# Performance work log

Hardware: AMD Instinct MI355X
Metric: run time of the kernel (lower is better)

The kernel has to match this reference:

```python
import jax, jax.numpy as jnp
import numpy as np

T, B, NA = 32, 32, 5          # timesteps, envs, actions
HID, FEAT = 256, 512          # lstm hidden, cnn features
IN_DIM = FEAT + NA            # lstm input size (517)
FLAT = 64 * 7 * 7             # cnn flatten size (3136)


def _conv(x, w, b, s):
    # x: NCHW, w: OIHW, VALID padding, stride s
    y = jax.lax.conv_general_dilated(x, w, (s, s), 'VALID',
                                     dimension_numbers=('NCHW', 'OIHW', 'NCHW'))
    return y + b[None, :, None, None]


def setup_inputs() -> dict:
    key = jax.random.key(0)
    ks = jax.random.split(key, 24)
    p = lambda k, shape: (jax.random.normal(k, shape, jnp.float32) * 0.05)
    return {
        'image': jax.random.uniform(ks[0], (T * B, 3, 84, 84), jnp.float32) * 255.0,
        'last_action': jax.random.randint(ks[1], (T * B,), 0, NA),
        'done': jax.random.bernoulli(ks[2], 0.05, (T * B,)).astype(jnp.float32),
        'h0': jnp.zeros((B, HID), jnp.float32),
        'c0': jnp.zeros((B, HID), jnp.float32),
        # NatureCNN params
        'W1': p(ks[3], (32, 3, 8, 8)), 'b1': jnp.zeros((32,), jnp.float32),
        'W2': p(ks[4], (64, 32, 4, 4)), 'b2': jnp.zeros((64,), jnp.float32),
        'W3': p(ks[5], (64, 64, 3, 3)), 'b3': jnp.zeros((64,), jnp.float32),
        'Wfc': p(ks[6], (FEAT, FLAT)), 'bfc': jnp.zeros((FEAT,), jnp.float32),
        # LSTM params (torch gate order i,f,g,o)
        'W_ih': p(ks[7], (4 * HID, IN_DIM)), 'W_hh': p(ks[8], (4 * HID, HID)),
        'b_ih': jnp.zeros((4 * HID,), jnp.float32), 'b_hh': jnp.zeros((4 * HID,), jnp.float32),
        # policy MLP (hidden 64, tanh)
        'Wp1': p(ks[9], (64, HID)), 'bp1': jnp.zeros((64,), jnp.float32),
        'Wp2': p(ks[10], (NA, 64)) * 0.01, 'bp2': jnp.zeros((NA,), jnp.float32),
        # value MLP
        'Wv1': p(ks[11], (64, HID)), 'bv1': jnp.zeros((64,), jnp.float32),
        'Wv2': p(ks[12], (1, 64)), 'bv2': jnp.zeros((1,), jnp.float32),
    }


def reference(image, last_action, done, h0, c0,
              W1, b1, W2, b2, W3, b3, Wfc, bfc,
              W_ih, W_hh, b_ih, b_hh,
              Wp1, bp1, Wp2, bp2, Wv1, bv1, Wv2, bv2):
    # --- extract: NatureCNN + one-hot(last_action) ---
    x = image / 255.0
    x = jax.nn.relu(_conv(x, W1, b1, 4))   # (TB,32,20,20)
    x = jax.nn.relu(_conv(x, W2, b2, 2))   # (TB,64,9,9)
    x = jax.nn.relu(_conv(x, W3, b3, 1))   # (TB,64,7,7)
    x = x.reshape(x.shape[0], -1)
    feat = jax.nn.relu(x @ Wfc.T + bfc)    # (TB,512)
    oh = jax.nn.one_hot(last_action, NA, dtype=feat.dtype)
    xs = jnp.concatenate([feat, oh], axis=1).reshape(T, B, IN_DIM)
    ds = done.reshape(T, B)

    # --- remember: done-masked LSTM recurrence (torch gate order i,f,g,o) ---
    def step(carry, inp):
        h, c = carry
        xt, dt = inp
        m = (1.0 - dt)[:, None]
        h = h * m
        c = c * m
        g = xt @ W_ih.T + b_ih + h @ W_hh.T + b_hh   # (B, 4*HID)
        i, f, gg, o = jnp.split(g, 4, axis=1)
        c = jax.nn.sigmoid(f) * c + jax.nn.sigmoid(i) * jnp.tanh(gg)
        h = jax.nn.sigmoid(o) * jnp.tanh(c)
        return (h, c), h

    (hT, cT), hs = jax.lax.scan(step, (h0, c0), (xs, ds))
    h = hs.reshape(T * B, HID)

    # --- heads ---
    logits = jnp.tanh(h @ Wp1.T + bp1) @ Wp2.T + bp2   # (TB, NA)
    v = jnp.tanh(h @ Wv1.T + bv1) @ Wv2.T + bv2        # (TB, 1)
    return logits, v, hT, cT
```

## Files before the change

kernel.cpp:

```cpp
#include <hip/hip_runtime.h>
#include <math.h>

typedef float  f4v __attribute__((ext_vector_type(4)));
typedef short  s8v __attribute__((ext_vector_type(8)));
typedef int    i4v __attribute__((ext_vector_type(4)));

__device__ __forceinline__ float sigm(float x) { return 1.f / (1.f + expf(-x)); }
__device__ __forceinline__ unsigned short f2bf(float f) {
    unsigned int u = __float_as_uint(f);
    return (unsigned short)((u + 0x7FFF + ((u >> 16) & 1)) >> 16);
}
__device__ __forceinline__ unsigned int cvt2(float lo, float hi) {
    unsigned int r;
    asm("v_cvt_pk_bf16_f32 %0, %1, %2" : "=v"(r) : "v"(lo), "v"(hi));
    return r;
}
__device__ __forceinline__ s8v pack8(float4 a, float4 b) {
    union { unsigned int u[4]; s8v v; } r;
    r.u[0] = cvt2(a.x, a.y); r.u[1] = cvt2(a.z, a.w);
    r.u[2] = cvt2(b.x, b.y); r.u[3] = cvt2(b.z, b.w);
    return r.v;
}
__device__ __forceinline__ void gload16(const void* g, void* l) {
    __builtin_amdgcn_global_load_lds((const __attribute__((address_space(1))) void*)g,
                                     (__attribute__((address_space(3))) void*)l, 16, 0, 0);
}

__global__ __launch_bounds__(256) void k_amax(const float* __restrict__ Whh,
                                              unsigned int* __restrict__ amax_bits) {
    int i = blockIdx.x * 256 + threadIdx.x;
    float v = fabsf(Whh[i]);
#pragma unroll
    for (int o = 1; o < 64; o <<= 1) v = fmaxf(v, __shfl_xor(v, o));
    if ((threadIdx.x & 63) == 0) atomicMax(amax_bits, __float_as_uint(v));
}

__global__ __launch_bounds__(256) void k_prep(const float* __restrict__ W2, const float* __restrict__ W3,
                                              const float* __restrict__ Wfc, const float* __restrict__ Wih,
                                              const float* __restrict__ W1, const float* __restrict__ Whh,
                                              const unsigned int* __restrict__ amax_bits,
                                              unsigned short* __restrict__ W2p, unsigned short* __restrict__ W3p,
                                              unsigned short* __restrict__ Wfcp, unsigned short* __restrict__ Wihp,
                                              unsigned short* __restrict__ W1p, signed char* __restrict__ Wq) {
    int i = blockIdx.x * 256 + threadIdx.x;
    if (i < 32768) {
        int co = i >> 9, k = i & 511, t = k >> 5, ci = k & 31, ky = t >> 2, kx = t & 3;
        W2p[i] = f2bf(W2[co * 512 + ci * 16 + ky * 4 + kx]);
    } else if (i < 69632) {
        int j = i - 32768;
        int co = j / 576, k = j - co * 576, t = k >> 6, ci = k & 63;
        int ky = t / 3, kx = t - ky * 3;
        W3p[j] = f2bf(W3[((co * 64 + ci) * 3 + ky) * 3 + kx]);
    } else if (i < 1675264) {
        int j = i - 69632;
        Wfcp[j] = f2bf(Wfc[j]);
    } else if (i < 2199552) {
        int j = i - 1675264;
        int n = j >> 9, k = j & 511;
        Wihp[j] = f2bf(Wih[n * 517 + k]);
    } else if (i < 2205696) {
        int j = i - 2199552;
        W1p[j] = f2bf(W1[j] * (1.f / 255.f));
    } else if (i < 2467840) {
        int j = i - 2205696;
        float amax = __uint_as_float(amax_bits[0]);
        float s = 127.f / amax;
        int qv = (int)rintf(Whh[j] * s);
        qv = qv > 127 ? 127 : (qv < -127 ? -127 : qv);
        Wq[j] = (signed char)qv;
    }
}

__global__ __launch_bounds__(256, 3) void k_conv1(const float* __restrict__ img,
                                                  const unsigned short* __restrict__ Bw,
                                                  const float* __restrict__ bias,
                                                  unsigned short* __restrict__ out) {
    __shared__ float sF[12096];
    int tid = threadIdx.x;
    int lane = tid & 63, w = tid >> 6;
    int l15 = lane & 15, q = lane >> 4;
    int bh = blockIdx.x & 1;
    int im = blockIdx.x >> 1;
    const int y0    = bh ? 40 : 0;
    const int S     = bh ? 14784 : 16128;
    const int fullc = bh ? 14 : 15;
    const int tailg = bh ? 28 : 48;
    const int t0    = bh ? 13 : 0;
    const int nt    = bh ? 12 : 13;
    char* sFb = (char*)sF;
    const char* gimg = (const char*)(img + (size_t)im * 21168);
    for (int c = 0; c < 3; ++c) {
        const char* gb = gimg + c * 28224 + y0 * 336;
        char* lb = sFb + c * S;
        for (int j = w; j < fullc; j += 4) {
            int off = j * 1024 + lane * 16;
            gload16(gb + off, lb + off);
        }
        if (w == c && lane < tailg) {
            int off = fullc * 1024 + lane * 16;
            *(float4*)(lb + off) = *(const float4*)(gb + off);
        }
    }
    const unsigned short* Bp0 = Bw + l15 * 192 + q * 8;
    const unsigned short* Bp1 = Bw + (16 + l15) * 192 + q * 8;
    s8v bf0[6], bf1[6];
#pragma unroll
    for (int ks = 0; ks < 6; ++ks) {
        bf0[ks] = *(const s8v*)(Bp0 + ks * 32);
        bf1[ks] = *(const s8v*)(Bp1 + ks * 32);
    }
    int koff[6];
#pragma unroll
    for (int ks = 0; ks < 6; ++ks) {
        int kq = ks * 4 + q;
        int c = kq >> 3, ky = kq & 7;
        koff[ks] = c * S + ky * 336;
    }
    __syncthreads();
    f4v acc[4][2];
#pragma unroll
    for (int i = 0; i < 4; ++i) { acc[i][0] = (f4v){0.f,0.f,0.f,0.f}; acc[i][1] = (f4v){0.f,0.f,0.f,0.f}; }
#pragma unroll
    for (int tt = 0; tt < 4; ++tt) {
        int li = w + tt * 4;
        if (li < nt) {
            int p = (t0 + li) * 16 + l15;
            int oy = p / 20, ox = p - oy * 20;
            int tb = (oy * 4 - y0) * 336 + ox * 16;
#pragma unroll
            for (int ks = 0; ks < 6; ++ks) {
                float4 a0 = *(const float4*)(sFb + koff[ks] + tb);
                float4 a1 = *(const float4*)(sFb + koff[ks] + tb + 16);
                s8v ua = pack8(a0, a1);
                acc[tt][0] = __builtin_amdgcn_mfma_f32_16x16x32_bf16(ua, bf0[ks], acc[tt][0], 0, 0, 0);
                acc[tt][1] = __builtin_amdgcn_mfma_f32_16x16x32_bf16(ua, bf1[ks], acc[tt][1], 0, 0, 0);
            }
        }
    }
    __syncthreads();
    unsigned short* cS = (unsigned short*)sFb;
    float b0v = bias[l15], b1v = bias[16 + l15];
#pragma unroll
    for (int tt = 0; tt < 4; ++tt) {
        int li = w + tt * 4;
        if (li < nt) {
            int pc = li * 16 + q * 4;
#pragma unroll
            for (int r = 0; r < 4; r += 2) {
                float v0 = acc[tt][0][r] + b0v;     v0 = v0 > 0.f ? v0 : 0.f;
                float v1 = acc[tt][0][r + 1] + b0v; v1 = v1 > 0.f ? v1 : 0.f;
                *(unsigned int*)&cS[l15 * 212 + pc + r] = cvt2(v0, v1);
                float u0 = acc[tt][1][r] + b1v;     u0 = u0 > 0.f ? u0 : 0.f;
                float u1 = acc[tt][1][r + 1] + b1v; u1 = u1 > 0.f ? u1 : 0.f;
                *(unsigned int*)&cS[(16 + l15) * 212 + pc + r] = cvt2(u0, u1);
            }
        }
    }
    __syncthreads();
    int hc = nt * 8;
    const unsigned int* cw = (const unsigned int*)cS;
    for (int n = w; n < 32; n += 4) {
        const unsigned int* crow = cw + n * 106;
        unsigned int* orow = (unsigned int*)(out + (im * 32 + n) * 400 + t0 * 16);
        for (int j = lane; j < hc; j += 64) orow[j] = crow[j];
    }
}

__global__ __launch_bounds__(256, 2) void k_conv2(const unsigned short* __restrict__ A,
                                                  const unsigned short* __restrict__ Bw,
                                                  const float* __restrict__ bias,
                                                  unsigned short* __restrict__ out) {
    __shared__ unsigned short sA[800 * 32];
    __shared__ unsigned short c2s[64][196];
    int tid = threadIdx.x;
    int lane = tid & 63, w = tid >> 6;
    int l15 = lane & 15, q = lane >> 4;
    int img0 = blockIdx.x * 2;
    char* sAb = (char*)sA;
    const s8v* srcv = (const s8v*)(A + img0 * 12800);
    for (int wi = tid; wi < 3200; wi += 256) {
        s8v v = srcv[wi];
        int f = wi * 8;
        int im = f / 12800, r = f - im * 12800, ci = r / 400, p = r - ci * 400;
#pragma unroll
        for (int j = 0; j < 8; ++j) {
            int R = im * 400 + p + j;
            int Rl = (R >> 1) + (R & 1) * 400;
            int by = (Rl * 32 + ci) * 2 ^ ((Rl & 7) << 4);
            *(unsigned short*)(sAb + by) = (unsigned short)v[j];
        }
    }
    __syncthreads();
    int Rb[3];
#pragma unroll
    for (int mf = 0; mf < 3; ++mf) {
        int t = w * 3 + mf;
        int im = t / 6;
        int pp = (t - im * 6) * 16 + l15;
        int px = pp > 80 ? 80 : pp;
        int oy = px / 9, ox = px - oy * 9;
        Rb[mf] = im * 400 + oy * 40 + ox * 2;
    }
    const unsigned short* Bp0 = Bw + l15 * 512 + q * 8;
    const unsigned short* Bp1 = Bw + (16 + l15) * 512 + q * 8;
    const unsigned short* Bp2 = Bw + (32 + l15) * 512 + q * 8;
    const unsigned short* Bp3 = Bw + (48 + l15) * 512 + q * 8;
    f4v acc[3][4];
#pragma unroll
    for (int i = 0; i < 3; ++i)
#pragma unroll
        for (int j = 0; j < 4; ++j) acc[i][j] = (f4v){0.f, 0.f, 0.f, 0.f};
#pragma unroll
    for (int s = 0; s < 16; ++s) {
        const int ky = s >> 2, kx = s & 3;
        const int d = ky * 20 + kx;
        s8v a[3];
#pragma unroll
        for (int mf = 0; mf < 3; ++mf) {
            int R = Rb[mf] + d;
            int Rl = (R >> 1) + (R & 1) * 400;
            int by = (Rl * 64 + q * 16) ^ ((Rl & 7) << 4);
            a[mf] = *(const s8v*)(sAb + by);
        }
        s8v b0 = *(const s8v*)(Bp0 + s * 32);
        s8v b1 = *(const s8v*)(Bp1 + s * 32);
        s8v b2 = *(const s8v*)(Bp2 + s * 32);
        s8v b3 = *(const s8v*)(Bp3 + s * 32);
#pragma unroll
        for (int mf = 0; mf < 3; ++mf) {
            acc[mf][0] = __builtin_amdgcn_mfma_f32_16x16x32_bf16(a[mf], b0, acc[mf][0], 0, 0, 0);
            acc[mf][1] = __builtin_amdgcn_mfma_f32_16x16x32_bf16(a[mf], b1, acc[mf][1], 0, 0, 0);
            acc[mf][2] = __builtin_amdgcn_mfma_f32_16x16x32_bf16(a[mf], b2, acc[mf][2], 0, 0, 0);
            acc[mf][3] = __builtin_amdgcn_mfma_f32_16x16x32_bf16(a[mf], b3, acc[mf][3], 0, 0, 0);
        }
    }
#pragma unroll
    for (int nf = 0; nf < 4; ++nf) {
        int co = nf * 16 + l15;
        float b = bias[co];
#pragma unroll
        for (int mf = 0; mf < 3; ++mf) {
            int rr = (w * 3 + mf) * 16 + q * 4;
#pragma unroll
            for (int r = 0; r < 4; r += 2) {
                float v0 = acc[mf][nf][r] + b;     v0 = v0 > 0.f ? v0 : 0.f;
                float v1 = acc[mf][nf][r + 1] + b; v1 = v1 > 0.f ? v1 : 0.f;
                *(unsigned int*)&c2s[co][rr + r] = cvt2(v0, v1);
            }
        }
    }
    __syncthreads();
    for (int idx = tid; idx < 10368; idx += 256) {
        int im = idx / 5184, r2 = idx - im * 5184, co = r2 / 81, p = r2 - co * 81;
        out[(img0 + im) * 5184 + r2] = c2s[co][im * 96 + p];
    }
}

__global__ __launch_bounds__(256, 2) void k_conv3(const unsigned short* __restrict__ A,
                                                  const unsigned short* __restrict__ Bw,
                                                  const float* __restrict__ bias,
                                                  unsigned short* __restrict__ out) {
    __shared__ unsigned short sA[162 * 64];
    __shared__ unsigned short c3s[64][132];
    int tid = threadIdx.x;
    int lane = tid & 63, w = tid >> 6;
    int l15 = lane & 15, q = lane >> 4;
    int img0 = blockIdx.x * 2;
    char* sAb = (char*)sA;
    const s8v* srcv = (const s8v*)(A + img0 * 5184);
    for (int wi = tid; wi < 1296; wi += 256) {
        s8v v = srcv[wi];
        int f = wi * 8;
#pragma unroll
        for (int j = 0; j < 8; ++j) {
            int fe = f + j;
            int im = fe / 5184, r = fe - im * 5184, ci = r / 81, p = r - ci * 81;
            int R = im * 81 + p;
            int by = (R * 64 + ci) * 2 ^ ((R & 7) << 4);
            *(unsigned short*)(sAb + by) = (unsigned short)v[j];
        }
    }
    __syncthreads();
    int Rb[2];
#pragma unroll
    for (int mf = 0; mf < 2; ++mf) {
        int t = w * 2 + mf;
        int im = t >> 2;
        int pp = (t & 3) * 16 + l15;
        int px = pp > 48 ? 48 : pp;
        int oy = px / 7, ox = px - oy * 7;
        Rb[mf] = im * 81 + oy * 9 + ox;
    }
    const unsigned short* Bp0 = Bw + l15 * 576 + q * 8;
    const unsigned short* Bp1 = Bw + (16 + l15) * 576 + q * 8;
    const unsigned short* Bp2 = Bw + (32 + l15) * 576 + q * 8;
    const unsigned short* Bp3 = Bw + (48 + l15) * 576 + q * 8;
    f4v acc[2][4];
#pragma unroll
    for (int i = 0; i < 2; ++i)
#pragma unroll
        for (int j = 0; j < 4; ++j) acc[i][j] = (f4v){0.f, 0.f, 0.f, 0.f};
#pragma unroll
    for (int s = 0; s < 18; ++s) {
        const int tap = s >> 1, cb2 = (s & 1) * 64;
        const int ky = tap / 3, kx = tap - ky * 3;
        const int d = ky * 9 + kx;
        s8v a0, a1;
        {
            int R = Rb[0] + d;
            int by = (R * 128 + cb2 + q * 16) ^ ((R & 7) << 4);
            a0 = *(const s8v*)(sAb + by);
        }
        {
            int R = Rb[1] + d;
            int by = (R * 128 + cb2 + q * 16) ^ ((R & 7) << 4);
            a1 = *(const s8v*)(sAb + by);
        }
        s8v b0 = *(const s8v*)(Bp0 + s * 32);
        s8v b1 = *(const s8v*)(Bp1 + s * 32);
        s8v b2 = *(const s8v*)(Bp2 + s * 32);
        s8v b3 = *(const s8v*)(Bp3 + s * 32);
        acc[0][0] = __builtin_amdgcn_mfma_f32_16x16x32_bf16(a0, b0, acc[0][0], 0, 0, 0);
        acc[0][1] = __builtin_amdgcn_mfma_f32_16x16x32_bf16(a0, b1, acc[0][1], 0, 0, 0);
        acc[0][2] = __builtin_amdgcn_mfma_f32_16x16x32_bf16(a0, b2, acc[0][2], 0, 0, 0);
        acc[0][3] = __builtin_amdgcn_mfma_f32_16x16x32_bf16(a0, b3, acc[0][3], 0, 0, 0);
        acc[1][0] = __builtin_amdgcn_mfma_f32_16x16x32_bf16(a1, b0, acc[1][0], 0, 0, 0);
        acc[1][1] = __builtin_amdgcn_mfma_f32_16x16x32_bf16(a1, b1, acc[1][1], 0, 0, 0);
        acc[1][2] = __builtin_amdgcn_mfma_f32_16x16x32_bf16(a1, b2, acc[1][2], 0, 0, 0);
        acc[1][3] = __builtin_amdgcn_mfma_f32_16x16x32_bf16(a1, b3, acc[1][3], 0, 0, 0);
    }
#pragma unroll
    for (int nf = 0; nf < 4; ++nf) {
        int co = nf * 16 + l15;
        float b = bias[co];
#pragma unroll
        for (int mf = 0; mf < 2; ++mf) {
            int rr = (w * 2 + mf) * 16 + q * 4;
#pragma unroll
            for (int r = 0; r < 4; r += 2) {
                float v0 = acc[mf][nf][r] + b;     v0 = v0 > 0.f ? v0 : 0.f;
                float v1 = acc[mf][nf][r + 1] + b; v1 = v1 > 0.f ? v1 : 0.f;
                *(unsigned int*)&c3s[co][rr + r] = cvt2(v0, v1);
            }
        }
    }
    __syncthreads();
    for (int idx = tid; idx < 6272; idx += 256) {
        int im = idx / 3136, r2 = idx - im * 3136, co = r2 / 49, p = r2 - co * 49;
        out[(img0 + im) * 3136 + r2] = c3s[co][im * 64 + p];
    }
}

__global__ __launch_bounds__(256) void k_fc(const unsigned short* __restrict__ A,
                                            const unsigned short* __restrict__ Bw,
                                            const float* __restrict__ bias,
                                            unsigned short* __restrict__ out) {
    int lane = threadIdx.x & 63, w = threadIdx.x >> 6;
    int l15 = lane & 15, q = lane >> 4;
    int m0 = blockIdx.x * 32 + (w & 1) * 16;
    int n0 = blockIdx.y * 64 + (w >> 1) * 32;
    const unsigned short* Ap = A + (m0 + l15) * 3136 + q * 8;
    const unsigned short* B0 = Bw + (n0 + l15) * 3136 + q * 8;
    const unsigned short* B1 = B0 + 16 * 3136;
    f4v acc0 = (f4v){0.f, 0.f, 0.f, 0.f}, acc1 = (f4v){0.f, 0.f, 0.f, 0.f};
    s8v av = *(const s8v*)Ap, b0 = *(const s8v*)B0, b1 = *(const s8v*)B1;
    for (int c = 0; c < 97; ++c) {
        Ap += 32; B0 += 32; B1 += 32;
        s8v nav = *(const s8v*)Ap, nb0 = *(const s8v*)B0, nb1 = *(const s8v*)B1;
        acc0 = __builtin_amdgcn_mfma_f32_16x16x32_bf16(av, b0, acc0, 0, 0, 0);
        acc1 = __builtin_amdgcn_mfma_f32_16x16x32_bf16(av, b1, acc1, 0, 0, 0);
        av = nav; b0 = nb0; b1 = nb1;
    }
    acc0 = __builtin_amdgcn_mfma_f32_16x16x32_bf16(av, b0, acc0, 0, 0, 0);
    acc1 = __builtin_amdgcn_mfma_f32_16x16x32_bf16(av, b1, acc1, 0, 0, 0);
    float bi0 = bias[n0 + l15], bi1 = bias[n0 + 16 + l15];
#pragma unroll
    for (int r = 0; r < 4; ++r) {
        int m = m0 + q * 4 + r;
        float v0 = acc0[r] + bi0; v0 = v0 > 0.f ? v0 : 0.f;
        float v1 = acc1[r] + bi1; v1 = v1 > 0.f ? v1 : 0.f;
        out[m * 512 + n0 + l15] = f2bf(v0);
        out[m * 512 + n0 + 16 + l15] = f2bf(v1);
    }
}

__global__ __launch_bounds__(256) void k_gx(const unsigned short* __restrict__ A,
                                            const unsigned short* __restrict__ Bw,
                                            const float* __restrict__ Wih,
                                            const float* __restrict__ bih,
                                            const float* __restrict__ bhh,
                                            const int* __restrict__ act,
                                            float* __restrict__ out) {
    int lane = threadIdx.x & 63, w = threadIdx.x >> 6;
    int l15 = lane & 15, q = lane >> 4;
    int m0 = blockIdx.x * 32 + (w & 1) * 16;
    int n0 = blockIdx.y * 64 + (w >> 1) * 32;
    const unsigned short* Ap = A + (m0 + l15) * 512 + q * 8;
    const unsigned short* B0 = Bw + (n0 + l15) * 512 + q * 8;
    const unsigned short* B1 = B0 + 16 * 512;
    f4v acc0 = (f4v){0.f, 0.f, 0.f, 0.f}, acc1 = (f4v){0.f, 0.f, 0.f, 0.f};
    for (int c = 0; c < 16; ++c) {
        s8v av = *(const s8v*)Ap;
        s8v b0 = *(const s8v*)B0;
        s8v b1 = *(const s8v*)B1;
        Ap += 32; B0 += 32; B1 += 32;
        acc0 = __builtin_amdgcn_mfma_f32_16x16x32_bf16(av, b0, acc0, 0, 0, 0);
        acc1 = __builtin_amdgcn_mfma_f32_16x16x32_bf16(av, b1, acc1, 0, 0, 0);
    }
    int na = n0 + l15, nb = n0 + 16 + l15;
    float ca = bih[na] + bhh[na], cb_ = bih[nb] + bhh[nb];
#pragma unroll
    for (int r = 0; r < 4; ++r) {
        int m = m0 + q * 4 + r;
        int a = act[m];
        out[m * 1024 + na] = acc0[r] + Wih[na * 517 + 512 + a] + ca;
        out[m * 1024 + nb] = acc1[r] + Wih[nb * 517 + 512 + a] + cb_;
    }
}

__global__ __launch_bounds__(1024) void k_lstm_all(const float* __restrict__ h0,
                                                   const float* __restrict__ c0,
                                                   const float* __restrict__ done,
                                                   const float* __restrict__ gx,
                                                   const signed char* __restrict__ Wq,
                                                   const unsigned int* __restrict__ amax_bits,
                                                   float* __restrict__ hs,
                                                   float* __restrict__ cb) {
    int b = blockIdx.x;
    int tid = threadIdx.x;
    int w = tid >> 6, lane = tid & 63;
    int l15 = lane & 15, q = lane >> 4;
    __shared__ float gbuf[1024];
    __shared__ float cst[256];
    __shared__ signed char hA[4][64][16];

    i4v wfr[4][4];
    const signed char* wb = Wq + (w * 64 + l15) * 256 + q * 16;
#pragma unroll
    for (int s = 0; s < 4; ++s)
#pragma unroll
        for (int kf = 0; kf < 4; ++kf)
            wfr[s][kf] = *(const i4v*)(wb + s * 16 * 256 + kf * 64);
    float sw = __uint_as_float(amax_bits[0]) * (1.f / (127.f * 127.f));

    ((int*)hA)[tid] = 0;
    __syncthreads();
    if (tid < 256) {
        int u = tid;
        cst[u] = c0[b * 256 + u];
        float m0v = 1.f - done[b];
        float hv = h0[b * 256 + u] * m0v;
        hv = hv > 1.f ? 1.f : (hv < -1.f ? -1.f : hv);
        hA[u >> 6][((u >> 4) & 3) * 16][u & 15] = (signed char)(int)rintf(hv * 127.f);
    }
    __syncthreads();

    for (int t = 0; t < 32; ++t) {
        float gxi = 0.f, gxf = 0.f, gxg = 0.f, gxo = 0.f, dcur = 0.f, dnxt = 0.f;
        if (tid < 256) {
            const float* gr = gx + (t * 32 + b) * 1024;
            gxi = gr[tid]; gxf = gr[256 + tid]; gxg = gr[512 + tid]; gxo = gr[768 + tid];
            dcur = done[t * 32 + b];
            dnxt = (t < 31) ? done[(t + 1) * 32 + b] : 1.f;
        }
        i4v acc[4];
#pragma unroll
        for (int s = 0; s < 4; ++s) acc[s] = (i4v){0, 0, 0, 0};
#pragma unroll
        for (int kf = 0; kf < 4; ++kf) {
            i4v a = *(const i4v*)&hA[kf][lane][0];
#pragma unroll
            for (int s = 0; s < 4; ++s)
                acc[s] = __builtin_amdgcn_mfma_i32_16x16x64_i8(a, wfr[s][kf], acc[s], 0, 0, 0);
        }
        if (q == 0) {
#pragma unroll
            for (int s = 0; s < 4; ++s)
                gbuf[w * 64 + s * 16 + l15] = (float)acc[s][0];
        }
        __syncthreads();
        if (tid < 256) {
            int u = tid;
            float gi = gbuf[u] * sw + gxi;
            float gf = gbuf[256 + u] * sw + gxf;
            float gg = gbuf[512 + u] * sw + gxg;
            float go = gbuf[768 + u] * sw + gxo;
            float cm = cst[u] * (1.f - dcur);
            float cn = sigm(gf) * cm + sigm(gi) * tanhf(gg);
            float hn = sigm(go) * tanhf(cn);
            cst[u] = cn;
            hs[t * 8192 + b * 256 + u] = hn;
            float hv = hn * (1.f - dnxt);
            hA[u >> 6][((u >> 4) & 3) * 16][u & 15] = (signed char)(int)rintf(hv * 127.f);
        }
        __syncthreads();
    }
    if (tid < 256) cb[b * 256 + tid] = cst[tid];
}

__global__ __launch_bounds__(256) void k_heads(const float* __restrict__ hs,
                                               const float* __restrict__ cb,
                                               const float* __restrict__ Wp1, const float* __restrict__ bp1,
                                               const float* __restrict__ Wp2, const float* __restrict__ bp2,
                                               const float* __restrict__ Wv1, const float* __restrict__ bv1,
                                               const float* __restrict__ Wv2, const float* __restrict__ bv2,
                                               float* __restrict__ out) {
    int lane = threadIdx.x & 63;
    int m = blockIdx.x * 4 + (threadIdx.x >> 6);
    const float4* hv = (const float4*)(hs + m * 256);
    const float4* wp = (const float4*)(Wp1 + lane * 256);
    const float4* wq = (const float4*)(Wv1 + lane * 256);
    float ap = 0.f, av = 0.f;
#pragma unroll 8
    for (int k = 0; k < 64; ++k) {
        float4 h4 = hv[k];
        float4 p4 = wp[k];
        float4 q4 = wq[k];
        ap += h4.x * p4.x + h4.y * p4.y + h4.z * p4.z + h4.w * p4.w;
        av += h4.x * q4.x + h4.y * q4.y + h4.z * q4.z + h4.w * q4.w;
    }
    float hp = tanhf(ap + bp1[lane]);
    float hq = tanhf(av + bv1[lane]);
#pragma unroll
    for (int j = 0; j < 5; ++j) {
        float s = hp * Wp2[j * 64 + lane];
        s += __shfl_xor(s, 1); s += __shfl_xor(s, 2); s += __shfl_xor(s, 4);
        s += __shfl_xor(s, 8); s += __shfl_xor(s, 16); s += __shfl_xor(s, 32);
        if (lane == 0) out[m * 5 + j] = s + bp2[j];
    }
    float s = hq * Wv2[lane];
    s += __shfl_xor(s, 1); s += __shfl_xor(s, 2); s += __shfl_xor(s, 4);
    s += __shfl_xor(s, 8); s += __shfl_xor(s, 16); s += __shfl_xor(s, 32);
    if (lane == 0) out[5120 + m] = s + bv2[0];

    int g = blockIdx.x * 256 + threadIdx.x;
    if (g < 8192) {
        out[6144 + g] = hs[31 * 8192 + g];
        out[6144 + 8192 + g] = cb[g];
    }
}

extern "C" void kernel_launch(void* const* d_in, const int* in_sizes, int n_in,
                              void* d_out, int out_size, void* d_ws, size_t ws_size,
                              hipStream_t stream) {
    const float* image = (const float*)d_in[0];
    const int*   act   = (const int*)d_in[1];
    const float* done  = (const float*)d_in[2];
    const float* h0    = (const float*)d_in[3];
    const float* c0    = (const float*)d_in[4];
    const float* W1    = (const float*)d_in[5];
    const float* b1    = (const float*)d_in[6];
    const float* W2    = (const float*)d_in[7];
    const float* b2    = (const float*)d_in[8];
    const float* W3    = (const float*)d_in[9];
    const float* b3    = (const float*)d_in[10];
    const float* Wfc   = (const float*)d_in[11];
    const float* bfc   = (const float*)d_in[12];
    const float* Wih   = (const float*)d_in[13];
    const float* Whh   = (const float*)d_in[14];
    const float* bih   = (const float*)d_in[15];
    const float* bhh   = (const float*)d_in[16];
    const float* Wp1   = (const float*)d_in[17];
    const float* bp1   = (const float*)d_in[18];
    const float* Wp2   = (const float*)d_in[19];
    const float* bp2   = (const float*)d_in[20];
    const float* Wv1   = (const float*)d_in[21];
    const float* bv1   = (const float*)d_in[22];
    const float* Wv2   = (const float*)d_in[23];
    const float* bv2   = (const float*)d_in[24];
    float* out = (float*)d_out;
    char* base = (char*)d_ws;

    unsigned short* a1   = (unsigned short*)(base);
    unsigned short* a2   = (unsigned short*)(base + 26214432);
    unsigned short* W2p  = (unsigned short*)(base + 36831328);
    unsigned short* W3p  = (unsigned short*)(base + 36896864);
    unsigned short* Wfcp = (unsigned short*)(base + 36970592);
    unsigned short* Wihp = (unsigned short*)(base + 40181856);
    unsigned short* W1p  = (unsigned short*)(base + 41230432);
    unsigned int*   amax = (unsigned int*)(base + 41242752);
    signed char*    Wq   = (signed char*)(base + 41242784);
    unsigned short* a3   = (unsigned short*)(base);
    unsigned short* feat = (unsigned short*)(base + 6422528);
    float* gx = (float*)(base + 7471104);
    float* hs = (float*)(base + 11665408);
    float* cb = (float*)(base + 12713984);

    hipMemsetAsync(amax, 0, 4, stream);
    k_amax<<<1024, 256, 0, stream>>>(Whh, amax);
    k_prep<<<9640, 256, 0, stream>>>(W2, W3, Wfc, Wih, W1, Whh, amax, W2p, W3p, Wfcp, Wihp, W1p, Wq);
    k_conv1<<<2048, 256, 0, stream>>>(image, W1p, b1, a1);
    k_conv2<<<512, 256, 0, stream>>>(a1, W2p, b2, a2);
    k_conv3<<<512, 256, 0, stream>>>(a2, W3p, b3, a3);
    k_fc<<<dim3(32, 8), 256, 0, stream>>>(a3, Wfcp, bfc, feat);
    k_gx<<<dim3(32, 16), 256, 0, stream>>>(feat, Wihp, Wih, bih, bhh, act, gx);
    k_lstm_all<<<32, 1024, 0, stream>>>(h0, c0, done, gx, Wq, amax, hs, cb);
    k_heads<<<256, 256, 0, stream>>>(hs, cb, Wp1, bp1, Wp2, bp2, Wv1, bv1, Wv2, bv2, out);
}
```

Baseline: 416.4 us.

## Stage FC and gate-input GEMM tiles through swizzled LDS with 8-wave blocks

Rewrites the FC and input-gate GEMM kernels so each 512-thread block cooperatively loads 32x128 A and 64x128 B tiles into XOR-swizzled shared memory. The eight waves each compute one 16x16 output fragment from those shared tiles instead of streaming global loads per wave. This is meant to raise memory-level parallelism and let tiles be reused across waves without LDS bank conflicts. In exchange it adds two barriers per K step, gives up the old register double-buffering, and the tail K step needs special-case loading.

Measured after the change: 397.8 us. 1.05x faster.

```diff
diff --git a/kernel.cpp b/kernel.cpp
--- a/kernel.cpp
+++ b/kernel.cpp
@@ -351,70 +351,126 @@
     }
 }
 
-__global__ __launch_bounds__(256) void k_fc(const unsigned short* __restrict__ A,
+__global__ __launch_bounds__(512) void k_fc(const unsigned short* __restrict__ A,
                                             const unsigned short* __restrict__ Bw,
                                             const float* __restrict__ bias,
                                             unsigned short* __restrict__ out) {
-    int lane = threadIdx.x & 63, w = threadIdx.x >> 6;
+    __shared__ unsigned short sA[32 * 128];
+    __shared__ unsigned short sB[64 * 128];
+    int tid = threadIdx.x;
+    int lane = tid & 63, w = tid >> 6;
     int l15 = lane & 15, q = lane >> 4;
-    int m0 = blockIdx.x * 32 + (w & 1) * 16;
-    int n0 = blockIdx.y * 64 + (w >> 1) * 32;
-    const unsigned short* Ap = A + (m0 + l15) * 3136 + q * 8;
-    const unsigned short* B0 = Bw + (n0 + l15) * 3136 + q * 8;
-    const unsigned short* B1 = B0 + 16 * 3136;
-    f4v acc0 = (f4v){0.f, 0.f, 0.f, 0.f}, acc1 = (f4v){0.f, 0.f, 0.f, 0.f};
-    s8v av = *(const s8v*)Ap, b0 = *(const s8v*)B0, b1 = *(const s8v*)B1;
-    for (int c = 0; c < 97; ++c) {
-        Ap += 32; B0 += 32; B1 += 32;
-        s8v nav = *(const s8v*)Ap, nb0 = *(const s8v*)B0, nb1 = *(const s8v*)B1;
-        acc0 = __builtin_amdgcn_mfma_f32_16x16x32_bf16(av, b0, acc0, 0, 0, 0);
-        acc1 = __builtin_amdgcn_mfma_f32_16x16x32_bf16(av, b1, acc1, 0, 0, 0);
-        av = nav; b0 = nb0; b1 = nb1;
-    }
-    acc0 = __builtin_amdgcn_mfma_f32_16x16x32_bf16(av, b0, acc0, 0, 0, 0);
-    acc1 = __builtin_amdgcn_mfma_f32_16x16x32_bf16(av, b1, acc1, 0, 0, 0);
-    float bi0 = bias[n0 + l15], bi1 = bias[n0 + 16 + l15];
+    int m0 = blockIdx.x * 32, n0 = blockIdx.y * 64;
+    int mh = w & 1, nh = w >> 1;
+    char* sAb = (char*)sA; char* sBb = (char*)sB;
+    int ar = mh * 16 + l15;
+    int br = nh * 16 + l15;
+    f4v acc = (f4v){0.f, 0.f, 0.f, 0.f};
+    for (int ks = 0; ks < 25; ++ks) {
+        int kb = ks * 128;
+        if (ks < 24) {
+            {
+                int row = tid >> 4, kg = tid & 15;
+                s8v v = *(const s8v*)(A + (m0 + row) * 3136 + kb + kg * 8);
+                int by = (row * 256 + kg * 16) ^ ((row & 7) << 4);
+                *(s8v*)(sAb + by) = v;
+            }
+#pragma unroll
+            for (int h = 0; h < 2; ++h) {
+                int g = tid + h * 512;
+                int row = g >> 4, kg = g & 15;
+                s8v v = *(const s8v*)(Bw + (n0 + row) * 3136 + kb + kg * 8);
+                int by = (row * 256 + kg * 16) ^ ((row & 7) << 4);
+                *(s8v*)(sBb + by) = v;
+            }
+        } else {
+            if (tid < 256) {
+                int row = tid >> 3, kg = tid & 7;
+                s8v v = *(const s8v*)(A + (m0 + row) * 3136 + kb + kg * 8);
+                int by = (row * 256 + kg * 16) ^ ((row & 7) << 4);
+                *(s8v*)(sAb + by) = v;
+            }
+            {
+                int row = tid >> 3, kg = tid & 7;
+                s8v v = *(const s8v*)(Bw + (n0 + row) * 3136 + kb + kg * 8);
+                int by = (row * 256 + kg * 16) ^ ((row & 7) << 4);
+                *(s8v*)(sBb + by) = v;
+            }
+        }
+        __syncthreads();
+        int nkc = (ks < 24) ? 4 : 2;
+        for (int kc = 0; kc < nkc; ++kc) {
+            int abz = (ar * 256 + kc * 64 + q * 16) ^ ((ar & 7) << 4);
+            int bbz = (br * 256 + kc * 64 + q * 16) ^ ((br & 7) << 4);
+            s8v av = *(const s8v*)(sAb + abz);
+            s8v bv = *(const s8v*)(sBb + bbz);
+            acc = __builtin_amdgcn_mfma_f32_16x16x32_bf16(av, bv, acc, 0, 0, 0);
+        }
+        __syncthreads();
+    }
+    int n = n0 + nh * 16 + l15;
+    float bi = bias[n];
 #pragma unroll
     for (int r = 0; r < 4; ++r) {
-        int m = m0 + q * 4 + r;
-        float v0 = acc0[r] + bi0; v0 = v0 > 0.f ? v0 : 0.f;
-        float v1 = acc1[r] + bi1; v1 = v1 > 0.f ? v1 : 0.f;
-        out[m * 512 + n0 + l15] = f2bf(v0);
-        out[m * 512 + n0 + 16 + l15] = f2bf(v1);
-    }
-}
-
-__global__ __launch_bounds__(256) void k_gx(const unsigned short* __restrict__ A,
+        int m = m0 + mh * 16 + q * 4 + r;
+        float v = acc[r] + bi; v = v > 0.f ? v : 0.f;
+        out[m * 512 + n] = f2bf(v);
+    }
+}
+
+__global__ __launch_bounds__(512) void k_gx(const unsigned short* __restrict__ A,
                                             const unsigned short* __restrict__ Bw,
                                             const float* __restrict__ Wih,
                                             const float* __restrict__ bih,
                                             const float* __restrict__ bhh,
                                             const int* __restrict__ act,
                                             float* __restrict__ out) {
-    int lane = threadIdx.x & 63, w = threadIdx.x >> 6;
+    __shared__ unsigned short sA[32 * 128];
+    __shared__ unsigned short sB[64 * 128];
+    int tid = threadIdx.x;
+    int lane = tid & 63, w = tid >> 6;
     int l15 = lane & 15, q = lane >> 4;
-    int m0 = blockIdx.x * 32 + (w & 1) * 16;
-    int n0 = blockIdx.y * 64 + (w >> 1) * 32;
-    const unsigned short* Ap = A + (m0 + l15) * 512 + q * 8;
-    const unsigned short* B0 = Bw + (n0 + l15) * 512 + q * 8;
-    const unsigned short* B1 = B0 + 16 * 512;
-    f4v acc0 = (f4v){0.f, 0.f, 0.f, 0.f}, acc1 = (f4v){0.f, 0.f, 0.f, 0.f};
-    for (int c = 0; c < 16; ++c) {
-        s8v av = *(const s8v*)Ap;
-        s8v b0 = *(const s8v*)B0;
-        s8v b1 = *(const s8v*)B1;
-        Ap += 32; B0 += 32; B1 += 32;
-        acc0 = __builtin_amdgcn_mfma_f32_16x16x32_bf16(av, b0, acc0, 0, 0, 0);
-        acc1 = __builtin_amdgcn_mfma_f32_16x16x32_bf16(av, b1, acc1, 0, 0, 0);
-    }
-    int na = n0 + l15, nb = n0 + 16 + l15;
-    float ca = bih[na] + bhh[na], cb_ = bih[nb] + bhh[nb];
+    int m0 = blockIdx.x * 32, n0 = blockIdx.y * 64;
+    int mh = w & 1, nh = w >> 1;
+    char* sAb = (char*)sA; char* sBb = (char*)sB;
+    int ar = mh * 16 + l15;
+    int br = nh * 16 + l15;
+    f4v acc = (f4v){0.f, 0.f, 0.f, 0.f};
+#pragma unroll
+    for (int ks = 0; ks < 4; ++ks) {
+        int kb = ks * 128;
+        {
+            int row = tid >> 4, kg = tid & 15;
+            s8v v = *(const s8v*)(A + (m0 + row) * 512 + kb + kg * 8);
+            int by = (row * 256 + kg * 16) ^ ((row & 7) << 4);
+            *(s8v*)(sAb + by) = v;
+        }
+#pragma unroll
+        for (int h = 0; h < 2; ++h) {
+            int g = tid + h * 512;
+            int row = g >> 4, kg = g & 15;
+            s8v v = *(const s8v*)(Bw + (n0 + row) * 512 + kb + kg * 8);
+            int by = (row * 256 + kg * 16) ^ ((row & 7) << 4);
+            *(s8v*)(sBb + by) = v;
+        }
+        __syncthreads();
+#pragma unroll
+        for (int kc = 0; kc < 4; ++kc) {
+            int abz = (ar * 256 + kc * 64 + q * 16) ^ ((ar & 7) << 4);
+            int bbz = (br * 256 + kc * 64 + q * 16) ^ ((br & 7) << 4);
+            s8v av = *(const s8v*)(sAb + abz);
+            s8v bv = *(const s8v*)(sBb + bbz);
+            acc = __builtin_amdgcn_mfma_f32_16x16x32_bf16(av, bv, acc, 0, 0, 0);
+        }
+        __syncthreads();
+    }
+    int n = n0 + nh * 16 + l15;
+    float cbias = bih[n] + bhh[n];
 #pragma unroll
     for (int r = 0; r < 4; ++r) {
-        int m = m0 + q * 4 + r;
+        int m = m0 + mh * 16 + q * 4 + r;
         int a = act[m];
-        out[m * 1024 + na] = acc0[r] + Wih[na * 517 + 512 + a] + ca;
-        out[m * 1024 + nb] = acc1[r] + Wih[nb * 517 + 512 + a] + cb_;
+        out[m * 1024 + n] = acc[r] + Wih[n * 517 + 512 + a] + cbias;
     }
 }
 
@@ -592,8 +648,8 @@
     k_conv1<<<2048, 256, 0, stream>>>(image, W1p, b1, a1);
     k_conv2<<<512, 256, 0, stream>>>(a1, W2p, b2, a2);
     k_conv3<<<512, 256, 0, stream>>>(a2, W3p, b3, a3);
-    k_fc<<<dim3(32, 8), 256, 0, stream>>>(a3, Wfcp, bfc, feat);
-    k_gx<<<dim3(32, 16), 256, 0, stream>>>(feat, Wihp, Wih, bih, bhh, act, gx);
+    k_fc<<<dim3(32, 8), 512, 0, stream>>>(a3, Wfcp, bfc, feat);
+    k_gx<<<dim3(32, 16), 512, 0, stream>>>(feat, Wihp, Wih, bih, bhh, act, gx);
     k_lstm_all<<<32, 1024, 0, stream>>>(h0, c0, done, gx, Wq, amax, hs, cb);
     k_heads<<<256, 256, 0, stream>>>(hs, cb, Wp1, bp1, Wp2, bp2, Wv1, bv1, Wv2, bv2, out);
 }
```
